# Optimization experiments

Hardware: AMD Instinct MI355X
Metric: run time of the kernel (lower is better)

The kernel has to match this reference:

```python
import jax, jax.numpy as jnp
import numpy as np

B, C, Dz, Hh, Ww = 1, 128, 24, 24, 24
L = Dz * Hh * Ww
D_STATE = 16
D_CONV = 4
EXPAND = 2
D_INNER = EXPAND * C
DT_RANK = (C + 15) // 16  # ceil(d_model/16) = 8


def setup_inputs() -> dict:
    key = jax.random.key(0)
    ks = jax.random.split(key, 10)
    s = 0.02
    return {
        "x": jax.random.normal(ks[0], (B, C, Dz, Hh, Ww), dtype=jnp.float32),
        "ln_w": jnp.ones((C,), jnp.float32),
        "ln_b": jnp.zeros((C,), jnp.float32),
        "in_proj_w": s * jax.random.normal(ks[1], (2 * D_INNER, C), jnp.float32),
        "conv_w": s * jax.random.normal(ks[2], (D_INNER, D_CONV), jnp.float32),
        "conv_b": jnp.zeros((D_INNER,), jnp.float32),
        "x_proj_w": s * jax.random.normal(ks[3], (DT_RANK + 2 * D_STATE, D_INNER), jnp.float32),
        "dt_proj_w": s * jax.random.normal(ks[4], (D_INNER, DT_RANK), jnp.float32),
        "dt_proj_b": jax.random.uniform(ks[5], (D_INNER,), jnp.float32, -4.0, -2.0),
        "A_log": jnp.log(jnp.broadcast_to(jnp.arange(1, D_STATE + 1, dtype=jnp.float32), (D_INNER, D_STATE))),
        "D_param": jnp.ones((D_INNER,), jnp.float32),
        "out_proj_w": s * jax.random.normal(ks[6], (C, D_INNER), jnp.float32),
    }


def _mamba_forward(x, ln_w, ln_b, in_proj_w, conv_w, conv_b, x_proj_w,
                   dt_proj_w, dt_proj_b, A_log, D_param, out_proj_w):
    b, c, d, h, w = x.shape
    l = d * h * w
    tokens = x.reshape(b, c, l).transpose(0, 2, 1)  # (B,L,C)

    # LayerNorm over channel dim
    mu = jnp.mean(tokens, axis=-1, keepdims=True)
    var = jnp.var(tokens, axis=-1, keepdims=True)
    tn = (tokens - mu) * jax.lax.rsqrt(var + 1e-5) * ln_w + ln_b

    # in_proj -> x, z
    xz = jnp.einsum('blc,ec->ble', tn, in_proj_w)  # (B,L,2*d_inner)
    xs, z = jnp.split(xz, 2, axis=-1)

    # causal depthwise conv1d over L (kernel size D_CONV)
    xpad = jnp.pad(xs, ((0, 0), (D_CONV - 1, 0), (0, 0)))
    xc = conv_b
    xc = sum(xpad[:, k:k + l, :] * conv_w[:, k] for k in range(D_CONV)) + conv_b
    xa = jax.nn.silu(xc)  # (B,L,d_inner)

    # x_proj -> dt, B, C
    x_dbl = jnp.einsum('bld,ed->ble', xa, x_proj_w)
    dt_in = x_dbl[..., :DT_RANK]
    Bm = x_dbl[..., DT_RANK:DT_RANK + D_STATE]          # (B,L,d_state)
    Cm = x_dbl[..., DT_RANK + D_STATE:]                 # (B,L,d_state)
    dt = jax.nn.softplus(jnp.einsum('blr,dr->bld', dt_in, dt_proj_w) + dt_proj_b)

    A = -jnp.exp(A_log)  # (d_inner, d_state)

    def step(hst, inp):
        dt_t, B_t, C_t, x_t = inp  # (B,d_inner),(B,d_state),(B,d_state),(B,d_inner)
        dA = jnp.exp(dt_t[..., None] * A)                       # (B,d_inner,d_state)
        hst = dA * hst + (dt_t * x_t)[..., None] * B_t[:, None, :]
        y_t = jnp.einsum('bds,bs->bd', hst, C_t)
        return hst, y_t

    h0 = jnp.zeros((b, D_INNER, D_STATE), xa.dtype)
    xs_t = (dt.transpose(1, 0, 2), Bm.transpose(1, 0, 2), Cm.transpose(1, 0, 2), xa.transpose(1, 0, 2))
    _, ys = jax.lax.scan(step, h0, xs_t)
    y = ys.transpose(1, 0, 2) + xa * D_param  # (B,L,d_inner)

    y = y * jax.nn.silu(z)
    out = jnp.einsum('bld,cd->blc', y, out_proj_w)

    tokens = tokens + out
    return tokens.transpose(0, 2, 1).reshape(b, c, d, h, w)


def reference(x, ln_w, ln_b, in_proj_w, conv_w, conv_b, x_proj_w,
              dt_proj_w, dt_proj_b, A_log, D_param, out_proj_w):
    return _mamba_forward(x, ln_w, ln_b, in_proj_w, conv_w, conv_b, x_proj_w,
                          dt_proj_w, dt_proj_b, A_log, D_param, out_proj_w)
```

## Files before the change

### kernel.cpp

```cpp
#include <hip/hip_runtime.h>
#include <hip/hip_bf16.h>
#include <math.h>


constexpr int LQ = 13824;
constexpr int NC = 216;
constexpr int CH = 64;
constexpr int NB = 108;
constexpr int DI = 256;
constexpr int DS = 16;

typedef __attribute__((ext_vector_type(8))) short short8v;
typedef __attribute__((ext_vector_type(4))) float float4v;

__device__ __forceinline__ ushort f2bf(float f) {
  uint u = __float_as_uint(f);
  u += 0x7FFFu + ((u >> 16) & 1u);
  return (ushort)(u >> 16);
}
__device__ __forceinline__ float bf2f(ushort u) {
  return __uint_as_float(((uint)u) << 16);
}

template<int CTRL>
__device__ __forceinline__ float dpp_add(float x) {
  int y = __builtin_amdgcn_update_dpp(0, __float_as_int(x), CTRL, 0xF, 0xF, true);
  return x + __int_as_float(y);
}
__device__ __forceinline__ float quad_reduce(float t) {
  t = dpp_add<0xB1>(t);
  t = dpp_add<0x4E>(t);
  return t;
}
__device__ __forceinline__ float softplus_f(float x) {
  return (x > 20.f) ? x : log1pf(__expf(x));
}

__global__ __launch_bounds__(256) void prep_w2(const float* __restrict__ w_in,
    const float* __restrict__ w_xp, const float* __restrict__ w_dt,
    const float* __restrict__ w_out,
    ushort* __restrict__ b_in, ushort* __restrict__ b_xp2, ushort* __restrict__ b_out) {
  int idx = blockIdx.x * 256 + threadIdx.x;
  if (idx < 65536) {
    b_in[idx] = f2bf(w_in[idx]);
  } else if (idx < 65536 + 8192) {
    int j = idx - 65536; int r = j >> 8, k = j & 255;
    b_xp2[j] = f2bf(w_xp[(8 + r) * 256 + k]);
  } else if (idx < 65536 + 8192 + 65536) {
    int j = idx - (65536 + 8192); int d = j >> 8, k = j & 255;
    float acc = 0.f;
    #pragma unroll
    for (int r = 0; r < 8; ++r) acc += w_dt[d * 8 + r] * w_xp[r * 256 + k];
    b_xp2[8192 + j] = f2bf(acc);
  } else if (idx < 65536 + 8192 + 65536 + 8192) {
    b_xp2[73728 + (idx - 139264)] = 0;
  } else if (idx < 180224) {
    int j = idx - 147456;
    b_out[j] = f2bf(w_out[j]);
  }
}

__global__ __launch_bounds__(256) void ln_t(const float* __restrict__ x,
    const float* __restrict__ lnw, const float* __restrict__ lnb,
    ushort* __restrict__ tn) {
  __shared__ float red[64][8];
  __shared__ float stat[64][2];
  __shared__ ushort T[64][136];
  const int t = threadIdx.x;
  const int l = t & 63, q = t >> 6;
  const int l0 = blockIdx.x * 64;
  float sum = 0.f, sq = 0.f;
  #pragma unroll 8
  for (int cc = 0; cc < 32; ++cc) {
    int c = q * 32 + cc;
    float v = x[(size_t)c * LQ + l0 + l];
    sum += v; sq += v * v;
  }
  red[l][q] = sum; red[l][4 + q] = sq;
  __syncthreads();
  if (t < 64) {
    float s  = red[t][0] + red[t][1] + red[t][2] + red[t][3];
    float s2 = red[t][4] + red[t][5] + red[t][6] + red[t][7];
    float mu = s * (1.f / 128.f);
    float var = s2 * (1.f / 128.f) - mu * mu;
    stat[t][0] = mu; stat[t][1] = rsqrtf(var + 1e-5f);
  }
  __syncthreads();
  float mu = stat[l][0], rs = stat[l][1];
  #pragma unroll 8
  for (int cc = 0; cc < 32; ++cc) {
    int c = q * 32 + cc;
    float v = x[(size_t)c * LQ + l0 + l];
    T[l][c] = f2bf((v - mu) * rs * lnw[c] + lnb[c]);
  }
  __syncthreads();
  int row = t >> 2, seg = t & 3;
  #pragma unroll
  for (int j = 0; j < 4; ++j) {
    short8v v = *(const short8v*)&T[row][seg * 32 + j * 8];
    *(short8v*)&tn[(size_t)(l0 + row) * 128 + seg * 32 + j * 8] = v;
  }
}

template<int K, int MV, int BSTR, int CSTR>
__global__ __launch_bounds__(256) void gemm_tok(
    const ushort* __restrict__ Wb,
    const ushort* __restrict__ Act,
    ushort* __restrict__ Out) {
  constexpr int KO = K / 8;
  __shared__ ushort As[64 * K];
  __shared__ ushort Bs[128 * 64];
  const int tid = threadIdx.x;
  const int l0 = blockIdx.x * 128;
  const int m0 = blockIdx.y * 64;
  #pragma unroll
  for (int i = 0; i < (64 * KO) / 256; ++i) {
    int cid = i * 256 + tid;
    int m = cid / KO, oct = cid % KO;
    short8v v = *(const short8v*)&Wb[(size_t)(m0 + m) * K + oct * 8];
    *(short8v*)&As[m * K + ((oct ^ (m & 7)) * 8)] = v;
  }
  float4v acc[4][2];
  #pragma unroll
  for (int a = 0; a < 4; ++a)
    #pragma unroll
    for (int b = 0; b < 2; ++b) acc[a][b] = (float4v)0.f;
  const int w = tid >> 6, lane = tid & 63;
  const int r = lane & 15, g = lane >> 4;
  for (int k0 = 0; k0 < K; k0 += 64) {
    __syncthreads();
    #pragma unroll
    for (int i = 0; i < 4; ++i) {
      int cid = i * 256 + tid;
      int l = cid >> 3, oct = cid & 7;
      short8v v = *(const short8v*)&Act[(size_t)(l0 + l) * BSTR + k0 + oct * 8];
      *(short8v*)&Bs[l * 64 + ((oct ^ (l & 7)) * 8)] = v;
    }
    __syncthreads();
    #pragma unroll
    for (int kk = 0; kk < 2; ++kk) {
      short8v af[4], bfv[2];
      int ko = (k0 >> 3) + kk * 4 + g;
      #pragma unroll
      for (int mf = 0; mf < 4; ++mf) {
        int row = mf * 16 + r;
        af[mf] = *(const short8v*)&As[row * K + ((ko ^ (row & 7)) * 8)];
      }
      int kob = kk * 4 + g;
      #pragma unroll
      for (int nf = 0; nf < 2; ++nf) {
        int row = w * 32 + nf * 16 + r;
        bfv[nf] = *(const short8v*)&Bs[row * 64 + ((kob ^ (row & 7)) * 8)];
      }
      #pragma unroll
      for (int mf = 0; mf < 4; ++mf)
        #pragma unroll
        for (int nf = 0; nf < 2; ++nf)
          acc[mf][nf] = __builtin_amdgcn_mfma_f32_16x16x32_bf16(af[mf], bfv[nf], acc[mf][nf], 0, 0, 0);
    }
  }
  __syncthreads();
  #pragma unroll
  for (int mf = 0; mf < 4; ++mf) {
    #pragma unroll
    for (int nf = 0; nf < 2; ++nf) {
      int l = w * 32 + nf * 16 + r;
      int m = mf * 16 + g * 4;
      ushort u0 = f2bf(acc[mf][nf][0]), u1 = f2bf(acc[mf][nf][1]);
      ushort u2 = f2bf(acc[mf][nf][2]), u3 = f2bf(acc[mf][nf][3]);
      uint2 pk = make_uint2((uint)u0 | ((uint)u1 << 16), (uint)u2 | ((uint)u3 << 16));
      int oct = (m >> 3) ^ (l & 7);
      *(uint2*)&Bs[l * 64 + oct * 8 + (g & 1) * 4] = pk;
    }
  }
  __syncthreads();
  #pragma unroll
  for (int i = 0; i < 4; ++i) {
    int cid = i * 256 + tid;
    int row = cid >> 3, oct = cid & 7;
    if (oct * 8 < MV) {
      short8v v = *(const short8v*)&Bs[row * 64 + ((oct ^ (row & 7)) * 8)];
      *(short8v*)&Out[(size_t)(l0 + row) * CSTR + m0 + oct * 8] = v;
    }
  }
}

__global__ __launch_bounds__(256) void gemm_out_k(
    const ushort* __restrict__ Wb,
    const ushort* __restrict__ Yg,
    const float* __restrict__ X,
    float* __restrict__ Out) {
  __shared__ ushort Ay[128 * 64];
  __shared__ ushort Bw[64 * 64];
  const int tid = threadIdx.x;
  const int l0 = blockIdx.x * 128;
  const int c0 = blockIdx.y * 64;
  const int w = tid >> 6, lane = tid & 63;
  const int r = lane & 15, g = lane >> 4;
  float4v acc[2][4];
  #pragma unroll
  for (int a = 0; a < 2; ++a)
    #pragma unroll
    for (int b = 0; b < 4; ++b) acc[a][b] = (float4v)0.f;
  for (int k0 = 0; k0 < 256; k0 += 64) {
    __syncthreads();
    #pragma unroll
    for (int i = 0; i < 4; ++i) {
      int cid = i * 256 + tid;
      int row = cid >> 3, oct = cid & 7;
      int k = k0 + oct * 8;
      int slab = k >> 4, rem = k & 15;
      short8v va = *(const short8v*)&Yg[((size_t)slab * LQ + l0 + row) * 16 + rem];
      *(short8v*)&Ay[row * 64 + ((oct ^ (row & 7)) * 8)] = va;
    }
    #pragma unroll
    for (int i = 0; i < 2; ++i) {
      int cid = i * 256 + tid;
      int row = cid >> 3, oct = cid & 7;
      short8v vb = *(const short8v*)&Wb[(size_t)(c0 + row) * 256 + k0 + oct * 8];
      *(short8v*)&Bw[row * 64 + ((oct ^ (row & 7)) * 8)] = vb;
    }
    __syncthreads();
    #pragma unroll
    for (int kk = 0; kk < 2; ++kk) {
      int ko = kk * 4 + g;
      short8v af[2], bfv[4];
      #pragma unroll
      for (int mf = 0; mf < 2; ++mf) {
        int row = w * 32 + mf * 16 + r;
        af[mf] = *(const short8v*)&Ay[row * 64 + ((ko ^ (row & 7)) * 8)];
      }
      #pragma unroll
      for (int nf = 0; nf < 4; ++nf) {
        int row = nf * 16 + r;
        bfv[nf] = *(const short8v*)&Bw[row * 64 + ((ko ^ (row & 7)) * 8)];
      }
      #pragma unroll
      for (int mf = 0; mf < 2; ++mf)
        #pragma unroll
        for (int nf = 0; nf < 4; ++nf)
          acc[mf][nf] = __builtin_amdgcn_mfma_f32_16x16x32_bf16(af[mf], bfv[nf], acc[mf][nf], 0, 0, 0);
    }
  }
  #pragma unroll
  for (int mf = 0; mf < 2; ++mf) {
    #pragma unroll
    for (int nf = 0; nf < 4; ++nf) {
      int c = c0 + nf * 16 + r;
      int l = l0 + w * 32 + mf * 16 + g * 4;
      size_t off = (size_t)c * LQ + l;
      float4 rv = *(const float4*)&X[off];
      float4 o = make_float4(acc[mf][nf][0] + rv.x, acc[mf][nf][1] + rv.y,
                             acc[mf][nf][2] + rv.z, acc[mf][nf][3] + rv.w);
      *(float4*)&Out[off] = o;
    }
  }
}

__global__ __launch_bounds__(256) void conv2(const ushort* __restrict__ xz,
    const float* __restrict__ cw, const float* __restrict__ cb,
    ushort* __restrict__ xa) {
  const int tid = threadIdx.x;
  const int d0 = (tid & 31) * 8;
  const int l0 = blockIdx.x * 32 + (tid >> 5) * 4;
  float w0[8], w1[8], w2[8], w3[8], bb[8];
  #pragma unroll
  for (int j = 0; j < 8; ++j) {
    float4 wv = *(const float4*)&cw[(d0 + j) * 4];
    w0[j] = wv.x; w1[j] = wv.y; w2[j] = wv.z; w3[j] = wv.w;
    bb[j] = cb[d0 + j];
  }
  float rbuf[7][8];
  #pragma unroll
  for (int t = 0; t < 7; ++t) {
    int ls = l0 - 3 + t;
    if (ls >= 0) {
      short8v v = *(const short8v*)&xz[(size_t)ls * 512 + d0];
      #pragma unroll
      for (int j = 0; j < 8; ++j) rbuf[t][j] = bf2f((ushort)v[j]);
    } else {
      #pragma unroll
      for (int j = 0; j < 8; ++j) rbuf[t][j] = 0.f;
    }
  }
  #pragma unroll
  for (int i = 0; i < 4; ++i) {
    short8v ov;
    #pragma unroll
    for (int j = 0; j < 8; ++j) {
      float acc = bb[j] + w0[j] * rbuf[i][j] + w1[j] * rbuf[i + 1][j]
                        + w2[j] * rbuf[i + 2][j] + w3[j] * rbuf[i + 3][j];
      ov[j] = (short)f2bf(acc / (1.f + __expf(-acc)));
    }
    *(short8v*)&xa[(size_t)(l0 + i) * 256 + d0] = ov;
  }
}

__global__ __launch_bounds__(256) void scan1(const ushort* __restrict__ xdbl,
    const ushort* __restrict__ xa, const float* __restrict__ bias,
    const float* __restrict__ A_log, float* __restrict__ Stot, float* __restrict__ Hc,
    ushort* __restrict__ yloc) {
  __shared__ uint  duL[64 * 64];
  __shared__ float bcL[64 * 32];
  __shared__ ushort ylds[64 * 72];
  const int tid = threadIdx.x;
  const int c = blockIdx.x, dg = blockIdx.y;
  const int dloc = tid >> 2, sq = tid & 3;
  const int d = dg * 64 + dloc;
  const int lb = c * CH;
  float4v A, h;
  #pragma unroll
  for (int k = 0; k < 4; ++k) {
    A[k] = -__expf(A_log[d * 16 + sq * 4 + k]);
    h[k] = 0.f;
  }
  float S = 0.f;
  {
    const int doff = dg * 64 + sq * 16;
    const ushort* xr = xdbl + (size_t)(lb + dloc) * 320 + 32 + doff;
    const ushort* xar = xa + (size_t)(lb + dloc) * 256 + doff;
    short8v d0 = *(const short8v*)xr;
    short8v d1 = *(const short8v*)(xr + 8);
    short8v x0 = *(const short8v*)xar;
    short8v x1 = *(const short8v*)(xar + 8);
    uint pk[16];
    #pragma unroll
    for (int j = 0; j < 8; ++j) {
      float sp = softplus_f(bf2f((ushort)d0[j]) + bias[doff + j]);
      pk[j] = (uint)f2bf(sp) | ((uint)f2bf(sp * bf2f((ushort)x0[j])) << 16);
      float sp2 = softplus_f(bf2f((ushort)d1[j]) + bias[doff + 8 + j]);
      pk[8 + j] = (uint)f2bf(sp2) | ((uint)f2bf(sp2 * bf2f((ushort)x1[j])) << 16);
    }
    uint4* dst = (uint4*)&duL[dloc * 64 + sq * 16];
    #pragma unroll
    for (int j = 0; j < 4; ++j)
      dst[j] = make_uint4(pk[4 * j], pk[4 * j + 1], pk[4 * j + 2], pk[4 * j + 3]);
  }
  if (tid < 128) {
    int row = tid >> 1, half = tid & 1;
    const ushort* xr = xdbl + (size_t)(lb + row) * 320;
    short8v bv = *(const short8v*)(xr + half * 8);
    short8v cv = *(const short8v*)(xr + 16 + half * 8);
    float* bd = &bcL[row * 32 + half * 8];
    float* cd = &bcL[row * 32 + 16 + half * 8];
    #pragma unroll
    for (int j = 0; j < 8; ++j) {
      bd[j] = bf2f((ushort)bv[j]);
      cd[j] = bf2f((ushort)cv[j]);
    }
  }
  __syncthreads();
  #pragma unroll 4
  for (int i = 0; i < CH; ++i) {
    uint pv = duL[i * 64 + dloc];
    float dtv = __uint_as_float(pv << 16);
    float dxv = __uint_as_float(pv & 0xffff0000u);
    S += dtv;
    float4v Bv = *(const float4v*)&bcL[i * 32 + sq * 4];
    float4v Cv = *(const float4v*)&bcL[i * 32 + 16 + sq * 4];
    float t = 0.f;
    #pragma unroll
    for (int k = 0; k < 4; ++k) {
      float a = __expf(dtv * A[k]);
      h[k] = fmaf(a, h[k], dxv * Bv[k]);
      t = fmaf(h[k], Cv[k], t);
    }
    t = quad_reduce(t);
    if (sq == 0) ylds[i * 72 + dloc] = f2bf(t);
  }
  __syncthreads();
  {
    int slab = tid >> 6, row = tid & 63;
    short8v v0 = *(const short8v*)&ylds[row * 72 + slab * 16];
    short8v v1 = *(const short8v*)&ylds[row * 72 + slab * 16 + 8];
    ushort* dst = &yloc[((size_t)(dg * 4 + slab) * LQ + lb + row) * 16];
    *(short8v*)dst = v0;
    *(short8v*)(dst + 8) = v1;
  }
  *(float4*)&Hc[(size_t)(c * 256 + d) * 16 + sq * 4] = make_float4(h[0], h[1], h[2], h[3]);
  if (sq == 0) Stot[c * 256 + d] = S;
}

__global__ __launch_bounds__(256) void scan_combine(const float* __restrict__ Stot,
    const float* __restrict__ Hc, const float* __restrict__ A_log,
    float* __restrict__ Hin) {
  int t = blockIdx.x * 256 + threadIdx.x;
  int d = t >> 4;
  float A = -__expf(A_log[t]);
  float h = 0.f;
  for (int c = 0; c < NC; ++c) {
    Hin[c * 4096 + t] = h;
    float a = __expf(A * Stot[c * 256 + d]);
    h = a * h + Hc[c * 4096 + t];
  }
}

__global__ __launch_bounds__(256) void scan2(const ushort* __restrict__ xdbl,
    const ushort* __restrict__ xa, const ushort* __restrict__ xz,
    const float* __restrict__ bias, const float* __restrict__ A_log,
    const float* __restrict__ Dp, const float* __restrict__ Hin,
    ushort* __restrict__ yg) {
  __shared__ uint  dtp[32 * 64];
  __shared__ float cL[64 * 16];
  __shared__ float corr[64 * 68];
  const int tid = threadIdx.x;
  const int c = blockIdx.x, dg = blockIdx.y;
  const int dloc = tid >> 2, sq = tid & 3;
  const int d = dg * 64 + dloc;
  const int lb = c * CH;
  float4v A, hin;
  #pragma unroll
  for (int k = 0; k < 4; ++k) A[k] = -__expf(A_log[d * 16 + sq * 4 + k]);
  {
    float4 hv = *(const float4*)&Hin[(size_t)(c * 256 + d) * 16 + sq * 4];
    hin[0] = hv.x; hin[1] = hv.y; hin[2] = hv.z; hin[3] = hv.w;
  }
  float S = 0.f;
  {
    int rp = tid >> 3, seg = tid & 7;
    const int doff = dg * 64 + seg * 8;
    const ushort* xr0 = xdbl + (size_t)(lb + 2 * rp) * 320 + 32 + doff;
    short8v e0 = *(const short8v*)xr0;
    short8v e1 = *(const short8v*)(xr0 + 320);
    uint pk[8];
    #pragma unroll
    for (int j = 0; j < 8; ++j) {
      float spe = softplus_f(bf2f((ushort)e0[j]) + bias[doff + j]);
      float spo = softplus_f(bf2f((ushort)e1[j]) + bias[doff + j]);
      pk[j] = (uint)f2bf(spe) | ((uint)f2bf(spo) << 16);
    }
    uint4* dst = (uint4*)&dtp[rp * 64 + seg * 8];
    dst[0] = make_uint4(pk[0], pk[1], pk[2], pk[3]);
    dst[1] = make_uint4(pk[4], pk[5], pk[6], pk[7]);
  }
  if (tid < 128) {
    int row = tid >> 1, half = tid & 1;
    short8v cv = *(const short8v*)(xdbl + (size_t)(lb + row) * 320 + 16 + half * 8);
    float* cd = &cL[row * 16 + half * 8];
    #pragma unroll
    for (int j = 0; j < 8; ++j) cd[j] = bf2f((ushort)cv[j]);
  }
  __syncthreads();
  #pragma unroll 2
  for (int i2 = 0; i2 < CH / 2; ++i2) {
    uint pv = dtp[i2 * 64 + dloc];
    #pragma unroll
    for (int par = 0; par < 2; ++par) {
      float dtv = (par == 0) ? __uint_as_float(pv << 16)
                             : __uint_as_float(pv & 0xffff0000u);
      S += dtv;
      int i = i2 * 2 + par;
      float4v Cv = *(const float4v*)&cL[i * 16 + sq * 4];
      float t = 0.f;
      #pragma unroll
      for (int k = 0; k < 4; ++k)
        t = fmaf(__expf(A[k] * S), hin[k] * Cv[k], t);
      t = quad_reduce(t);
      if (sq == 0) corr[i * 68 + dloc] = t;
    }
  }
  __syncthreads();
  {
    int slab = tid >> 6, row = tid & 63;
    const int doff = dg * 64 + slab * 16;
    size_t sl = ((size_t)(dg * 4 + slab) * LQ + lb + row) * 16;
    short8v y0 = *(const short8v*)&yg[sl];
    short8v y1 = *(const short8v*)&yg[sl + 8];
    const ushort* xav = xa + (size_t)(lb + row) * 256 + doff;
    short8v x0 = *(const short8v*)xav;
    short8v x1 = *(const short8v*)(xav + 8);
    const ushort* zvp = xz + (size_t)(lb + row) * 512 + 256 + doff;
    short8v z0 = *(const short8v*)zvp;
    short8v z1 = *(const short8v*)(zvp + 8);
    float4 c0 = *(const float4*)&corr[row * 68 + slab * 16];
    float4 c1 = *(const float4*)&corr[row * 68 + slab * 16 + 4];
    float4 c2 = *(const float4*)&corr[row * 68 + slab * 16 + 8];
    float4 c3 = *(const float4*)&corr[row * 68 + slab * 16 + 12];
    float cr[16] = {c0.x, c0.y, c0.z, c0.w, c1.x, c1.y, c1.z, c1.w,
                    c2.x, c2.y, c2.z, c2.w, c3.x, c3.y, c3.z, c3.w};
    short8v o0, o1;
    #pragma unroll
    for (int j = 0; j < 8; ++j) {
      float v0 = bf2f((ushort)y0[j]) + cr[j] + bf2f((ushort)x0[j]) * Dp[doff + j];
      float zf0 = bf2f((ushort)z0[j]);
      o0[j] = (short)f2bf(v0 * (zf0 / (1.f + __expf(-zf0))));
      float v1 = bf2f((ushort)y1[j]) + cr[8 + j] + bf2f((ushort)x1[j]) * Dp[doff + 8 + j];
      float zf1 = bf2f((ushort)z1[j]);
      o1[j] = (short)f2bf(v1 * (zf1 / (1.f + __expf(-zf1))));
    }
    *(short8v*)&yg[sl] = o0;
    *(short8v*)&yg[sl + 8] = o1;
  }
}

extern "C" void kernel_launch(void* const* d_in, const int* in_sizes, int n_in,
                              void* d_out, int out_size, void* d_ws, size_t ws_size,
                              hipStream_t stream) {
  const float* x         = (const float*)d_in[0];
  const float* ln_w      = (const float*)d_in[1];
  const float* ln_b      = (const float*)d_in[2];
  const float* in_proj_w = (const float*)d_in[3];
  const float* conv_w    = (const float*)d_in[4];
  const float* conv_b    = (const float*)d_in[5];
  const float* x_proj_w  = (const float*)d_in[6];
  const float* dt_proj_w = (const float*)d_in[7];
  const float* dt_proj_b = (const float*)d_in[8];
  const float* A_log     = (const float*)d_in[9];
  const float* D_param   = (const float*)d_in[10];
  const float* out_proj_w= (const float*)d_in[11];
  float* out = (float*)d_out;

  char* ws = (char*)d_ws;
  ushort* wbf_in  = (ushort*)(ws + 0);
  ushort* wbf_xp2 = (ushort*)(ws + 131072);
  ushort* wbf_out = (ushort*)(ws + 294912);
  float*  Hin     = (float*)(ws + 360448);
  float*  Hc      = (float*)(ws + 3899392);
  float*  Stot    = (float*)(ws + 7438336);
  ushort* tn_t    = (ushort*)(ws + 7659520);
  ushort* xz_t    = (ushort*)(ws + 11198464);
  ushort* xa_t    = (ushort*)(ws + 25354240);
  ushort* xdbl_t  = (ushort*)(ws + 32432128);
  ushort* yg_t    = (ushort*)(ws + 41279488);

  prep_w2<<<704, 256, 0, stream>>>(in_proj_w, x_proj_w, dt_proj_w, out_proj_w,
                                   wbf_in, wbf_xp2, wbf_out);
  ln_t<<<LQ / 64, 256, 0, stream>>>(x, ln_w, ln_b, tn_t);
  gemm_tok<128, 64, 128, 512><<<dim3(NB, 8), 256, 0, stream>>>(wbf_in, tn_t, xz_t);
  conv2<<<LQ / 32, 256, 0, stream>>>(xz_t, conv_w, conv_b, xa_t);
  gemm_tok<256, 64, 256, 320><<<dim3(NB, 5), 256, 0, stream>>>(wbf_xp2, xa_t, xdbl_t);
  scan1<<<dim3(NC, 4), 256, 0, stream>>>(xdbl_t, xa_t, dt_proj_b, A_log, Stot, Hc, yg_t);
  scan_combine<<<16, 256, 0, stream>>>(Stot, Hc, A_log, Hin);
  scan2<<<dim3(NC, 4), 256, 0, stream>>>(xdbl_t, xa_t, xz_t, dt_proj_b, A_log,
                                         D_param, Hin, yg_t);
  gemm_out_k<<<dim3(NB, 2), 256, 0, stream>>>(wbf_out, yg_t, x, out);
}
```

Measured before the change: 203.3 us.

## Double-buffer GEMM activation tiles via direct global-to-LDS loads and batch scan_combine loads

Both token GEMMs now double-buffer the activation tile in LDS and prefetch the next K-slice with global_load_lds while the MFMAs run on the current one. This removes one barrier per iteration and overlaps memory latency with compute. The output GEMM also loads the whole 64x256 weight slice into LDS once at kernel start instead of reloading it every K step. scan_combine batches its loads eight chunks at a time so the serial recurrence is not stalled on each global load, at the cost of more LDS and registers.

```diff
diff --git a/kernel.cpp b/kernel.cpp
--- a/kernel.cpp
+++ b/kernel.cpp
@@ -20,6 +20,11 @@
 }
 __device__ __forceinline__ float bf2f(ushort u) {
   return __uint_as_float(((uint)u) << 16);
+}
+__device__ __forceinline__ void gl_lds16(const ushort* g, ushort* l) {
+  __builtin_amdgcn_global_load_lds(
+      (const __attribute__((address_space(1))) void*)g,
+      (__attribute__((address_space(3))) void*)l, 16, 0, 0);
 }
 
 template<int CTRL>
@@ -109,7 +114,7 @@
     ushort* __restrict__ Out) {
   constexpr int KO = K / 8;
   __shared__ ushort As[64 * K];
-  __shared__ ushort Bs[128 * 64];
+  __shared__ ushort Bs[2][128 * 64];
   const int tid = threadIdx.x;
   const int l0 = blockIdx.x * 128;
   const int m0 = blockIdx.y * 64;
@@ -120,6 +125,12 @@
     short8v v = *(const short8v*)&Wb[(size_t)(m0 + m) * K + oct * 8];
     *(short8v*)&As[m * K + ((oct ^ (m & 7)) * 8)] = v;
   }
+  #pragma unroll
+  for (int i = 0; i < 4; ++i) {
+    int cid = i * 256 + tid;
+    int l = cid >> 3, oct = (cid & 7) ^ (l & 7);
+    gl_lds16(&Act[(size_t)(l0 + l) * BSTR + oct * 8], &Bs[0][cid * 8]);
+  }
   float4v acc[4][2];
   #pragma unroll
   for (int a = 0; a < 4; ++a)
@@ -127,16 +138,19 @@
     for (int b = 0; b < 2; ++b) acc[a][b] = (float4v)0.f;
   const int w = tid >> 6, lane = tid & 63;
   const int r = lane & 15, g = lane >> 4;
+  int buf = 0;
+  __syncthreads();
   for (int k0 = 0; k0 < K; k0 += 64) {
-    __syncthreads();
-    #pragma unroll
-    for (int i = 0; i < 4; ++i) {
-      int cid = i * 256 + tid;
-      int l = cid >> 3, oct = cid & 7;
-      short8v v = *(const short8v*)&Act[(size_t)(l0 + l) * BSTR + k0 + oct * 8];
-      *(short8v*)&Bs[l * 64 + ((oct ^ (l & 7)) * 8)] = v;
-    }
-    __syncthreads();
+    if (k0 + 64 < K) {
+      #pragma unroll
+      for (int i = 0; i < 4; ++i) {
+        int cid = i * 256 + tid;
+        int l = cid >> 3, oct = (cid & 7) ^ (l & 7);
+        gl_lds16(&Act[(size_t)(l0 + l) * BSTR + (k0 + 64) + oct * 8],
+                 &Bs[buf ^ 1][cid * 8]);
+      }
+    }
+    const ushort* bp = Bs[buf];
     #pragma unroll
     for (int kk = 0; kk < 2; ++kk) {
       short8v af[4], bfv[2];
@@ -150,7 +164,7 @@
       #pragma unroll
       for (int nf = 0; nf < 2; ++nf) {
         int row = w * 32 + nf * 16 + r;
-        bfv[nf] = *(const short8v*)&Bs[row * 64 + ((kob ^ (row & 7)) * 8)];
+        bfv[nf] = *(const short8v*)&bp[row * 64 + ((kob ^ (row & 7)) * 8)];
       }
       #pragma unroll
       for (int mf = 0; mf < 4; ++mf)
@@ -158,8 +172,9 @@
         for (int nf = 0; nf < 2; ++nf)
           acc[mf][nf] = __builtin_amdgcn_mfma_f32_16x16x32_bf16(af[mf], bfv[nf], acc[mf][nf], 0, 0, 0);
     }
-  }
-  __syncthreads();
+    __syncthreads();
+    buf ^= 1;
+  }
   #pragma unroll
   for (int mf = 0; mf < 4; ++mf) {
     #pragma unroll
@@ -170,7 +185,7 @@
       ushort u2 = f2bf(acc[mf][nf][2]), u3 = f2bf(acc[mf][nf][3]);
       uint2 pk = make_uint2((uint)u0 | ((uint)u1 << 16), (uint)u2 | ((uint)u3 << 16));
       int oct = (m >> 3) ^ (l & 7);
-      *(uint2*)&Bs[l * 64 + oct * 8 + (g & 1) * 4] = pk;
+      *(uint2*)&Bs[0][l * 64 + oct * 8 + (g & 1) * 4] = pk;
     }
   }
   __syncthreads();
@@ -179,7 +194,7 @@
     int cid = i * 256 + tid;
     int row = cid >> 3, oct = cid & 7;
     if (oct * 8 < MV) {
-      short8v v = *(const short8v*)&Bs[row * 64 + ((oct ^ (row & 7)) * 8)];
+      short8v v = *(const short8v*)&Bs[0][row * 64 + ((oct ^ (row & 7)) * 8)];
       *(short8v*)&Out[(size_t)(l0 + row) * CSTR + m0 + oct * 8] = v;
     }
   }
@@ -190,50 +205,60 @@
     const ushort* __restrict__ Yg,
     const float* __restrict__ X,
     float* __restrict__ Out) {
-  __shared__ ushort Ay[128 * 64];
-  __shared__ ushort Bw[64 * 64];
+  __shared__ ushort Ay[2][128 * 64];
+  __shared__ ushort Bw[64 * 256];
   const int tid = threadIdx.x;
   const int l0 = blockIdx.x * 128;
   const int c0 = blockIdx.y * 64;
   const int w = tid >> 6, lane = tid & 63;
   const int r = lane & 15, g = lane >> 4;
+  #pragma unroll
+  for (int i = 0; i < 8; ++i) {
+    int cid = i * 256 + tid;
+    int row = cid >> 5, oct = cid & 31;
+    short8v vb = *(const short8v*)&Wb[(size_t)(c0 + row) * 256 + oct * 8];
+    *(short8v*)&Bw[row * 256 + ((oct ^ (row & 7)) * 8)] = vb;
+  }
+  #pragma unroll
+  for (int i = 0; i < 4; ++i) {
+    int cid = i * 256 + tid;
+    int row = cid >> 3, oct = (cid & 7) ^ (row & 7);
+    gl_lds16(&Yg[((size_t)(oct >> 1) * LQ + l0 + row) * 16 + (oct & 1) * 8],
+             &Ay[0][cid * 8]);
+  }
   float4v acc[2][4];
   #pragma unroll
   for (int a = 0; a < 2; ++a)
     #pragma unroll
     for (int b = 0; b < 4; ++b) acc[a][b] = (float4v)0.f;
+  int buf = 0;
+  __syncthreads();
   for (int k0 = 0; k0 < 256; k0 += 64) {
-    __syncthreads();
-    #pragma unroll
-    for (int i = 0; i < 4; ++i) {
-      int cid = i * 256 + tid;
-      int row = cid >> 3, oct = cid & 7;
-      int k = k0 + oct * 8;
-      int slab = k >> 4, rem = k & 15;
-      short8v va = *(const short8v*)&Yg[((size_t)slab * LQ + l0 + row) * 16 + rem];
-      *(short8v*)&Ay[row * 64 + ((oct ^ (row & 7)) * 8)] = va;
-    }
-    #pragma unroll
-    for (int i = 0; i < 2; ++i) {
-      int cid = i * 256 + tid;
-      int row = cid >> 3, oct = cid & 7;
-      short8v vb = *(const short8v*)&Wb[(size_t)(c0 + row) * 256 + k0 + oct * 8];
-      *(short8v*)&Bw[row * 64 + ((oct ^ (row & 7)) * 8)] = vb;
-    }
-    __syncthreads();
+    if (k0 + 64 < 256) {
+      int ks = (k0 + 64) >> 4;
+      #pragma unroll
+      for (int i = 0; i < 4; ++i) {
+        int cid = i * 256 + tid;
+        int row = cid >> 3, oct = (cid & 7) ^ (row & 7);
+        gl_lds16(&Yg[((size_t)(ks + (oct >> 1)) * LQ + l0 + row) * 16 + (oct & 1) * 8],
+                 &Ay[buf ^ 1][cid * 8]);
+      }
+    }
+    const ushort* ap = Ay[buf];
     #pragma unroll
     for (int kk = 0; kk < 2; ++kk) {
-      int ko = kk * 4 + g;
+      int kob = kk * 4 + g;
+      int ko = (k0 >> 3) + kob;
       short8v af[2], bfv[4];
       #pragma unroll
       for (int mf = 0; mf < 2; ++mf) {
         int row = w * 32 + mf * 16 + r;
-        af[mf] = *(const short8v*)&Ay[row * 64 + ((ko ^ (row & 7)) * 8)];
+        af[mf] = *(const short8v*)&ap[row * 64 + ((kob ^ (row & 7)) * 8)];
       }
       #pragma unroll
       for (int nf = 0; nf < 4; ++nf) {
         int row = nf * 16 + r;
-        bfv[nf] = *(const short8v*)&Bw[row * 64 + ((ko ^ (row & 7)) * 8)];
+        bfv[nf] = *(const short8v*)&Bw[row * 256 + ((ko ^ (row & 7)) * 8)];
       }
       #pragma unroll
       for (int mf = 0; mf < 2; ++mf)
@@ -241,6 +266,8 @@
         for (int nf = 0; nf < 4; ++nf)
           acc[mf][nf] = __builtin_amdgcn_mfma_f32_16x16x32_bf16(af[mf], bfv[nf], acc[mf][nf], 0, 0, 0);
     }
+    __syncthreads();
+    buf ^= 1;
   }
   #pragma unroll
   for (int mf = 0; mf < 2; ++mf) {
@@ -388,10 +415,18 @@
   int d = t >> 4;
   float A = -__expf(A_log[t]);
   float h = 0.f;
-  for (int c = 0; c < NC; ++c) {
-    Hin[c * 4096 + t] = h;
-    float a = __expf(A * Stot[c * 256 + d]);
-    h = a * h + Hc[c * 4096 + t];
+  for (int cb = 0; cb < NC; cb += 8) {
+    float a[8], b[8];
+    #pragma unroll
+    for (int j = 0; j < 8; ++j) {
+      a[j] = Stot[(cb + j) * 256 + d];
+      b[j] = Hc[(size_t)(cb + j) * 4096 + t];
+    }
+    #pragma unroll
+    for (int j = 0; j < 8; ++j) {
+      Hin[(size_t)(cb + j) * 4096 + t] = h;
+      h = fmaf(__expf(A * a[j]), h, b[j]);
+    }
   }
 }
 
```

New measurement: 201.2 us. Within noise of the previous version (-1.0%).
